# Performance work log

Measured on AMD Instinct MI355X. Metric: run time of the kernel, lower is better.

The kernel has to match this reference:

```python
import jax, jax.numpy as jnp
import numpy as np

N_NODES = 50000
N_EDGES = 1600000
IN_CH = 128
HID = 128
OUT_CH = 6
NUM_GRAPHS = 512


def _lin_params(key, fan_in, fan_out):
    k1, k2 = jax.random.split(key)
    bound = 1.0 / np.sqrt(fan_in)
    W = jax.random.uniform(k1, (fan_in, fan_out), minval=-bound, maxval=bound, dtype=jnp.float32)
    b = jax.random.uniform(k2, (fan_out,), minval=-bound, maxval=bound, dtype=jnp.float32)
    return W, b


def setup_inputs() -> dict:
    key = jax.random.key(0)
    ks = jax.random.split(key, 10)
    x = jax.random.normal(ks[0], (N_NODES, IN_CH), dtype=jnp.float32)
    edge_index = jax.random.randint(ks[1], (2, N_EDGES), 0, N_NODES, dtype=jnp.int64)
    batch = jnp.sort(jax.random.randint(ks[2], (N_NODES,), 0, NUM_GRAPHS, dtype=jnp.int64))
    W1a, b1a = _lin_params(ks[3], IN_CH, HID)
    W1b, b1b = _lin_params(ks[4], HID, HID)
    W2a, b2a = _lin_params(ks[5], HID, HID)
    W2b, b2b = _lin_params(ks[6], HID, HID)
    Wf1, bf1 = _lin_params(ks[7], HID, HID)
    Wf2, bf2 = _lin_params(ks[8], HID, OUT_CH)
    return {"x": x, "edge_index": edge_index, "batch": batch,
            "W1a": W1a, "b1a": b1a, "W1b": W1b, "b1b": b1b,
            "W2a": W2a, "b2a": b2a, "W2b": W2b, "b2b": b2b,
            "Wf1": Wf1, "bf1": bf1, "Wf2": Wf2, "bf2": bf2}


def _gin_conv(x, src, dst, Wa, ba, Wb, bb):
    # aggregate: sum of source-node features into target nodes (eps = 0)
    agg = jax.ops.segment_sum(x[src], dst, num_segments=N_NODES)
    h = x + agg  # (1 + eps) * x + sum_neighbors
    h = jax.nn.relu(h @ Wa + ba) @ Wb + bb  # 2-layer MLP (nn1/nn2)
    return h


def reference(x, edge_index, batch, W1a, b1a, W1b, b1b, W2a, b2a, W2b, b2b, Wf1, bf1, Wf2, bf2):
    src, dst = edge_index[0], edge_index[1]
    h = jax.nn.relu(_gin_conv(x, src, dst, W1a, b1a, W1b, b1b))
    h = jax.nn.relu(_gin_conv(h, src, dst, W2a, b2a, W2b, b2b))
    # global mean pool over graph ids
    sums = jax.ops.segment_sum(h, batch, num_segments=NUM_GRAPHS)  # [G, HID]
    counts = jax.ops.segment_sum(jnp.ones((h.shape[0],), h.dtype), batch, num_segments=NUM_GRAPHS)
    pooled = sums / jnp.maximum(counts, 1.0)[:, None]
    out = jax.nn.relu(pooled @ Wf1 + bf1) @ Wf2 + bf2  # [G, 6]
    return jax.nn.sigmoid(out)
```

## Files before the change

### kernel.cpp

```cpp
#include <hip/hip_runtime.h>

typedef unsigned short u16;
typedef unsigned int u32;

#define N_NODES 50000
#define N_EDGES 1600000
#define CH 128
#define CHW 64
#define NG 512
#define CAP 128
#define PAD 136
#define NBINS 196
#define BINCAP 12288
#define ECHUNK 1563

typedef __bf16 bf16x8 __attribute__((ext_vector_type(8)));
typedef float f32x4 __attribute__((ext_vector_type(4)));

#define OFF_DEG 0ull
#define OFF_BUCKET 200192ull
#define OFF_XB 13000192ull
#define OFF_HSUM 25800192ull
#define OFF_H1 38600192ull
#define OFF_GS 51400192ull
#define OFF_GE 51402240ull
#define OFF_BCUR 51404288ull
#define OFF_WT 51405312ull
#define OFF_BC 51536384ull
#define OFF_WF1 51538432ull
#define OFF_BF1 51603968ull
#define OFF_WF2 51604480ull
#define OFF_BF2 51607552ull

__device__ __forceinline__ float bflo(u32 v) { return __builtin_bit_cast(float, v << 16); }
__device__ __forceinline__ float bfhi(u32 v) { return __builtin_bit_cast(float, v & 0xffff0000u); }
__device__ __forceinline__ float bf2f(u16 v) { return __builtin_bit_cast(float, ((u32)v) << 16); }
__device__ __forceinline__ u16 f2bf(float f) {
    u32 x = __builtin_bit_cast(u32, f);
    x += 0x7fffu + ((x >> 16) & 1u);
    return (u16)(x >> 16);
}
__device__ __forceinline__ u32 pack2(float a, float b) {
    return (u32)f2bf(a) | ((u32)f2bf(b) << 16);
}
__device__ __forceinline__ bool probe_bf16(u32 w0) {
    u32 ex = (w0 >> 7) & 0xFFu;
    bool ok = ((w0 & 0x7FFFu) == 0u) || (ex >= 0x70u && ex <= 0x8Fu);
    return __popcll(__ballot(ok)) >= 48;
}
__device__ __forceinline__ float loadf(const void* p, int i, bool isbf) {
    return isbf ? bf2f(((const u16*)p)[i]) : ((const float*)p)[i];
}

__global__ __launch_bounds__(256) void fused_pre(char* ws, const u32* __restrict__ x,
                                                 u32* __restrict__ xb,
                                                 const int* __restrict__ ei,
                                                 const int* __restrict__ batch,
                                                 int* __restrict__ gstart, int* __restrict__ gend,
                                                 int* __restrict__ binCursor, u32* __restrict__ binned,
                                                 const void* W0, const void* W1,
                                                 const void* W2, const void* W3,
                                                 const void* b0, const void* b1,
                                                 const void* b2, const void* b3,
                                                 const void* Wf1, const void* bf1,
                                                 const void* Wf2, const void* bf2) {
    __shared__ __align__(16) char smem[33024];
    int tid = threadIdx.x, lane = tid & 63;
    int b = blockIdx.x;
    if (b < 8) {
        bool isbf = probe_bf16(((const u32*)W0)[lane]);
        int j = b >> 1, hf = b & 1;
        const void* src = (j == 0) ? W0 : (j == 1) ? W1 : (j == 2) ? W2 : W3;
        float* tile = (float*)smem;
        for (int it = 0; it < 32; ++it) {
            int idx = it * 256 + tid;
            int k = idx >> 7, n = idx & 127;
            tile[k * 129 + n] = loadf(src, (hf * 64 + k) * 128 + n, isbf);
        }
        __syncthreads();
        u16* Wt = (u16*)(ws + OFF_WT) + j * 16384;
        for (int it = 0; it < 32; ++it) {
            int o = it * 256 + tid;
            int n = o >> 6, kk = o & 63;
            Wt[n * 128 + hf * 64 + kk] = f2bf(tile[kk * 129 + n]);
        }
        return;
    }
    if (b < 78) {
        bool isbf = probe_bf16(((const u32*)W0)[lane]);
        int idx = (b - 8) * 256 + tid;
        float* bc = (float*)(ws + OFF_BC);
        float* Wf1c = (float*)(ws + OFF_WF1);
        float* bf1c = (float*)(ws + OFF_BF1);
        float* Wf2c = (float*)(ws + OFF_WF2);
        float* bf2c = (float*)(ws + OFF_BF2);
        if (idx < 512) {
            int j = idx >> 7, c = idx & 127;
            const void* src = (j == 0) ? b0 : (j == 1) ? b1 : (j == 2) ? b2 : b3;
            bc[idx] = loadf(src, c, isbf);
        } else if (idx < 16896) {
            Wf1c[idx - 512] = loadf(Wf1, idx - 512, isbf);
        } else if (idx < 17024) {
            bf1c[idx - 16896] = loadf(bf1, idx - 16896, isbf);
        } else if (idx < 17792) {
            Wf2c[idx - 17024] = loadf(Wf2, idx - 17024, isbf);
        } else if (idx < 17798) {
            bf2c[idx - 17792] = loadf(bf2, idx - 17792, isbf);
        }
        return;
    }
    if (b < 12578) {
        bool isbf = probe_bf16(x[lane]);
        int bb = b - 78;
        int i = bb * 256 + tid;
        if (isbf) {
            xb[i] = x[i];
        } else {
            float2 v = ((const float2*)x)[i];
            xb[i] = pack2(v.x, v.y);
        }
        if (bb < 196) {
            u32 hiw = ((const u32*)batch)[2 * (12500 + lane) + 1];
            bool i64 = __popcll(__ballot(hiw == 0u)) >= 48;
            int n = bb * 256 + tid;
            if (n < N_NODES) {
                int g = i64 ? batch[2 * n] : batch[n];
                atomicMin(&gstart[g], n);
                atomicMax(&gend[g], n + 1);
            }
        }
        return;
    }
    {
        int wg = b - 12578;
        u32* lhist = (u32*)smem;
        u32* lbase = lhist + 256;
        u32* lcur = lbase + 256;
        u32* stash = lcur + 256;
        u32 hiw = ((const u32*)ei)[2 * lane + 1];
        bool i64 = __popcll(__ballot(hiw == 0u)) >= 48;
        int e0 = wg * ECHUNK;
        int cnt = N_EDGES - e0; if (cnt > ECHUNK) cnt = ECHUNK; if (cnt < 0) cnt = 0;
        lhist[tid] = 0; lcur[tid] = 0;
        __syncthreads();
        for (int li = tid; li < cnt; li += 256) {
            int e = e0 + li;
            int s, d;
            if (i64) { s = ei[2 * e]; d = ei[2 * N_EDGES + 2 * e]; }
            else     { s = ei[e];     d = ei[N_EDGES + e]; }
            stash[li] = ((u32)d << 16) | (u32)s;
            atomicAdd(&lhist[d >> 8], 1u);
        }
        __syncthreads();
        u32 c = lhist[tid];
        if (c) lbase[tid] = (u32)atomicAdd(&binCursor[tid], (int)c);
        __syncthreads();
        for (int li = tid; li < cnt; li += 256) {
            u32 wv = stash[li];
            int bin = (int)(wv >> 24);
            u32 p = atomicAdd(&lcur[bin], 1u);
            binned[(size_t)bin * BINCAP + lbase[bin] + p] = wv;
        }
    }
}

__global__ __launch_bounds__(256) void fill_from_binned(const int* __restrict__ binCursor,
                                                        const u32* __restrict__ binned,
                                                        int* __restrict__ deg,
                                                        u16* __restrict__ bucket) {
    __shared__ u32 ldeg[256];
    int tid = threadIdx.x, b = blockIdx.x;
    int cnt = binCursor[b];
    ldeg[tid] = 0;
    __syncthreads();
    const u32* bp = binned + (size_t)b * BINCAP;
    for (int i = tid; i < cnt; i += 256) {
        u32 w = bp[i];
        u32 dl = (w >> 16) & 255u;
        u32 pos = atomicAdd(&ldeg[dl], 1u);
        if (pos < CAP) bucket[(size_t)(w >> 16) * CAP + pos] = (u16)(w & 0xFFFFu);
    }
    __syncthreads();
    int node = b * 256 + tid;
    if (node < N_NODES) deg[node] = (int)ldeg[tid];
}

__global__ __launch_bounds__(256) void agg_kernel(const u32* __restrict__ h,
                                                  const int* __restrict__ deg,
                                                  const u16* __restrict__ bucket,
                                                  u32* __restrict__ out) {
    int w = threadIdx.x >> 6, lane = threadIdx.x & 63;
    int node = blockIdx.x * 4 + w;
    if (node >= N_NODES) return;
    int sub = lane >> 4, q = lane & 15;
    const uint4* h4 = (const uint4*)h;
    float acc[8];
    {
        uint4 sv = make_uint4(0u, 0u, 0u, 0u);
        if (sub == 0) sv = h4[(size_t)node * 16 + q];
        acc[0] = bflo(sv.x); acc[1] = bfhi(sv.x);
        acc[2] = bflo(sv.y); acc[3] = bfhi(sv.y);
        acc[4] = bflo(sv.z); acc[5] = bfhi(sv.z);
        acc[6] = bflo(sv.w); acc[7] = bfhi(sv.w);
    }
    int d = deg[node];
    d = d > CAP ? CAP : d;
    const u32* bkw = (const u32*)(bucket + (size_t)node * CAP);
    const u32 sh = (u32)(sub & 1) * 16u;
    const int widx = sub >> 1;
    int j = 0;
    for (; j + 16 <= d; j += 16) {
        int base = j >> 1;
        u32 wd0 = bkw[base + widx];
        u32 wd1 = bkw[base + 2 + widx];
        u32 wd2 = bkw[base + 4 + widx];
        u32 wd3 = bkw[base + 6 + widx];
        uint4 v0 = h4[(size_t)((wd0 >> sh) & 0xFFFFu) * 16 + q];
        uint4 v1 = h4[(size_t)((wd1 >> sh) & 0xFFFFu) * 16 + q];
        uint4 v2 = h4[(size_t)((wd2 >> sh) & 0xFFFFu) * 16 + q];
        uint4 v3 = h4[(size_t)((wd3 >> sh) & 0xFFFFu) * 16 + q];
        acc[0] += bflo(v0.x) + bflo(v1.x) + bflo(v2.x) + bflo(v3.x);
        acc[1] += bfhi(v0.x) + bfhi(v1.x) + bfhi(v2.x) + bfhi(v3.x);
        acc[2] += bflo(v0.y) + bflo(v1.y) + bflo(v2.y) + bflo(v3.y);
        acc[3] += bfhi(v0.y) + bfhi(v1.y) + bfhi(v2.y) + bfhi(v3.y);
        acc[4] += bflo(v0.z) + bflo(v1.z) + bflo(v2.z) + bflo(v3.z);
        acc[5] += bfhi(v0.z) + bfhi(v1.z) + bfhi(v2.z) + bfhi(v3.z);
        acc[6] += bflo(v0.w) + bflo(v1.w) + bflo(v2.w) + bflo(v3.w);
        acc[7] += bfhi(v0.w) + bfhi(v1.w) + bfhi(v2.w) + bfhi(v3.w);
    }
    for (; j + 4 <= d; j += 4) {
        u32 wd = bkw[(j >> 1) + widx];
        uint4 v = h4[(size_t)((wd >> sh) & 0xFFFFu) * 16 + q];
        acc[0] += bflo(v.x); acc[1] += bfhi(v.x);
        acc[2] += bflo(v.y); acc[3] += bfhi(v.y);
        acc[4] += bflo(v.z); acc[5] += bfhi(v.z);
        acc[6] += bflo(v.w); acc[7] += bfhi(v.w);
    }
    if (j + sub < d) {
        int e = j + sub;
        u32 wd = bkw[e >> 1];
        u32 id = (wd >> ((u32)(e & 1) * 16u)) & 0xFFFFu;
        uint4 v = h4[(size_t)id * 16 + q];
        acc[0] += bflo(v.x); acc[1] += bfhi(v.x);
        acc[2] += bflo(v.y); acc[3] += bfhi(v.y);
        acc[4] += bflo(v.z); acc[5] += bfhi(v.z);
        acc[6] += bflo(v.w); acc[7] += bfhi(v.w);
    }
#pragma unroll
    for (int c = 0; c < 8; ++c) {
        acc[c] += __shfl_xor(acc[c], 16, 64);
        acc[c] += __shfl_xor(acc[c], 32, 64);
    }
    if (sub == 0) {
        uint4 o;
        o.x = pack2(acc[0], acc[1]);
        o.y = pack2(acc[2], acc[3]);
        o.z = pack2(acc[4], acc[5]);
        o.w = pack2(acc[6], acc[7]);
        ((uint4*)out)[(size_t)node * 16 + q] = o;
    }
}

__global__ __launch_bounds__(256) void mlp_kernel(const u16* __restrict__ in,
                                                  const u16* __restrict__ Wta,
                                                  const float* __restrict__ ba,
                                                  const u16* __restrict__ Wtb,
                                                  const float* __restrict__ bb,
                                                  u16* __restrict__ out,
                                                  int nrows) {
    __shared__ __align__(16) u16 Wlds[128 * PAD];
    __shared__ __align__(16) u16 tlds[64 * PAD];
    const int tid = threadIdx.x;
    const int w = tid >> 6;
    const int lane = tid & 63;
    const int n16 = lane & 15;
    const int quad = lane >> 4;
    const int row0 = blockIdx.x * 64 + w * 16;
    const bool active = row0 < nrows;

    {
        const uint4* wsrc = (const uint4*)Wta;
#pragma unroll
        for (int it = 0; it < 8; ++it) {
            int idx = tid + it * 256;
            int n = idx >> 4, c = idx & 15;
            *(uint4*)&Wlds[n * PAD + c * 8] = wsrc[idx];
        }
    }
    __syncthreads();

    f32x4 acc[8];
    bf16x8 afrag[4];
    if (active) {
        const u16* rowp = in + (size_t)(row0 + n16) * CH + quad * 8;
#pragma unroll
        for (int ks = 0; ks < 4; ++ks)
            afrag[ks] = *(const bf16x8*)(rowp + ks * 32);
#pragma unroll
        for (int ct = 0; ct < 8; ++ct) {
            f32x4 a = {0.f, 0.f, 0.f, 0.f};
#pragma unroll
            for (int ks = 0; ks < 4; ++ks) {
                bf16x8 b = *(const bf16x8*)&Wlds[(u32)(ct * 16 + n16) * PAD + ks * 32 + quad * 8];
                a = __builtin_amdgcn_mfma_f32_16x16x32_bf16(afrag[ks], b, a, 0, 0, 0);
            }
            acc[ct] = a;
        }
#pragma unroll
        for (int ct = 0; ct < 8; ++ct) {
            float bv = ba[ct * 16 + n16];
#pragma unroll
            for (int r = 0; r < 4; ++r) {
                float v = fmaxf(acc[ct][r] + bv, 0.f);
                tlds[(w * 16 + quad * 4 + r) * PAD + ct * 16 + n16] = f2bf(v);
            }
        }
    }
    __syncthreads();
    {
        const uint4* wsrc = (const uint4*)Wtb;
#pragma unroll
        for (int it = 0; it < 8; ++it) {
            int idx = tid + it * 256;
            int n = idx >> 4, c = idx & 15;
            *(uint4*)&Wlds[n * PAD + c * 8] = wsrc[idx];
        }
    }
    __syncthreads();

    if (active) {
#pragma unroll
        for (int ks = 0; ks < 4; ++ks)
            afrag[ks] = *(const bf16x8*)&tlds[(u32)(w * 16 + n16) * PAD + ks * 32 + quad * 8];
#pragma unroll
        for (int ct = 0; ct < 8; ++ct) {
            f32x4 a = {0.f, 0.f, 0.f, 0.f};
#pragma unroll
            for (int ks = 0; ks < 4; ++ks) {
                bf16x8 b = *(const bf16x8*)&Wlds[(u32)(ct * 16 + n16) * PAD + ks * 32 + quad * 8];
                a = __builtin_amdgcn_mfma_f32_16x16x32_bf16(afrag[ks], b, a, 0, 0, 0);
            }
            acc[ct] = a;
        }
#pragma unroll
        for (int ct = 0; ct < 8; ++ct) {
            float bv = bb[ct * 16 + n16];
#pragma unroll
            for (int r = 0; r < 4; ++r) {
                float v = fmaxf(acc[ct][r] + bv, 0.f);
                tlds[(w * 16 + quad * 4 + r) * PAD + ct * 16 + n16] = f2bf(v);
            }
        }
        u32* outw = (u32*)out;
        for (int r = 0; r < 16; ++r) {
            u32 v = *(const u32*)&tlds[(w * 16 + r) * PAD + lane * 2];
            outw[(size_t)(row0 + r) * CHW + lane] = v;
        }
    }
}

__global__ __launch_bounds__(256) void pool_final(const u32* __restrict__ h,
                                                  const int* __restrict__ gstart,
                                                  const int* __restrict__ gend,
                                                  const float* __restrict__ Wf1,
                                                  const float* __restrict__ bf1,
                                                  const float* __restrict__ Wf2,
                                                  const float* __restrict__ bf2v,
                                                  float* __restrict__ out) {
    __shared__ float rowb[4][128];
    __shared__ float tb[4][128];
    int w = threadIdx.x >> 6, lane = threadIdx.x & 63;
    int g = blockIdx.x * 4 + w;
    int sub = lane >> 4, q = lane & 15;
    int s = gstart[g], e = gend[g];
    const uint4* h4 = (const uint4*)h;
    float acc[8] = {0.f, 0.f, 0.f, 0.f, 0.f, 0.f, 0.f, 0.f};
    int i = s + sub;
    for (; i + 4 < e; i += 8) {
        uint4 v0 = h4[(size_t)i * 16 + q];
        uint4 v1 = h4[(size_t)(i + 4) * 16 + q];
        acc[0] += bflo(v0.x) + bflo(v1.x); acc[1] += bfhi(v0.x) + bfhi(v1.x);
        acc[2] += bflo(v0.y) + bflo(v1.y); acc[3] += bfhi(v0.y) + bfhi(v1.y);
        acc[4] += bflo(v0.z) + bflo(v1.z); acc[5] += bfhi(v0.z) + bfhi(v1.z);
        acc[6] += bflo(v0.w) + bflo(v1.w); acc[7] += bfhi(v0.w) + bfhi(v1.w);
    }
    for (; i < e; i += 4) {
        uint4 v = h4[(size_t)i * 16 + q];
        acc[0] += bflo(v.x); acc[1] += bfhi(v.x);
        acc[2] += bflo(v.y); acc[3] += bfhi(v.y);
        acc[4] += bflo(v.z); acc[5] += bfhi(v.z);
        acc[6] += bflo(v.w); acc[7] += bfhi(v.w);
    }
#pragma unroll
    for (int c = 0; c < 8; ++c) {
        acc[c] += __shfl_xor(acc[c], 16, 64);
        acc[c] += __shfl_xor(acc[c], 32, 64);
    }
    if (sub == 0) {
        float inv = 1.f / (float)((e - s) > 0 ? (e - s) : 1);
#pragma unroll
        for (int k = 0; k < 4; ++k) {
            rowb[w][(q * 4 + k) * 2] = acc[2 * k] * inv;
            rowb[w][(q * 4 + k) * 2 + 1] = acc[2 * k + 1] * inv;
        }
    }
    __syncthreads();
#pragma unroll
    for (int jj = 0; jj < 2; ++jj) {
        int jn = lane + jj * 64;
        float a = bf1[jn];
        for (int k = 0; k < 128; ++k) a += rowb[w][k] * Wf1[k * 128 + jn];
        tb[w][jn] = fmaxf(a, 0.f);
    }
    __syncthreads();
    if (lane < 6) {
        float a = bf2v[lane];
        for (int k = 0; k < 128; ++k) a += tb[w][k] * Wf2[k * 6 + lane];
        out[g * 6 + lane] = 1.f / (1.f + __expf(-a));
    }
}

extern "C" void kernel_launch(void* const* d_in, const int* in_sizes, int n_in,
                              void* d_out, int out_size, void* d_ws, size_t ws_size,
                              hipStream_t stream) {
    const u32* x = (const u32*)d_in[0];
    const int* ei = (const int*)d_in[1];
    const int* batch = (const int*)d_in[2];
    float* out = (float*)d_out;

    char* ws = (char*)d_ws;
    int* deg = (int*)(ws + OFF_DEG);
    u16* bucket = (u16*)(ws + OFF_BUCKET);
    u32* XB = (u32*)(ws + OFF_XB);
    u32* HSUM = (u32*)(ws + OFF_HSUM);
    u32* H1 = (u32*)(ws + OFF_H1);
    int* gstart = (int*)(ws + OFF_GS);
    int* gend = (int*)(ws + OFF_GE);
    int* binCursor = (int*)(ws + OFF_BCUR);
    u16* Wt = (u16*)(ws + OFF_WT);
    float* bc = (float*)(ws + OFF_BC);
    float* Wf1c = (float*)(ws + OFF_WF1);
    float* bf1c = (float*)(ws + OFF_BF1);
    float* Wf2c = (float*)(ws + OFF_WF2);
    float* bf2c = (float*)(ws + OFF_BF2);
    u32* binned = HSUM;

    hipMemsetAsync(gend, 0, 3072, stream);
    hipMemsetAsync(gstart, 0x7F, 2048, stream);

    fused_pre<<<13602, 256, 0, stream>>>(ws, x, XB, ei, batch, gstart, gend, binCursor, binned,
        d_in[3], d_in[5], d_in[7], d_in[9],
        d_in[4], d_in[6], d_in[8], d_in[10],
        d_in[11], d_in[12], d_in[13], d_in[14]);
    fill_from_binned<<<NBINS, 256, 0, stream>>>(binCursor, binned, deg, bucket);

    agg_kernel<<<(N_NODES + 3) / 4, 256, 0, stream>>>(XB, deg, bucket, HSUM);
    mlp_kernel<<<(N_NODES + 63) / 64, 256, 0, stream>>>((const u16*)HSUM, Wt, bc,
                                                        Wt + 16384, bc + 128, (u16*)H1, N_NODES);
    agg_kernel<<<(N_NODES + 3) / 4, 256, 0, stream>>>(H1, deg, bucket, HSUM);
    mlp_kernel<<<(N_NODES + 63) / 64, 256, 0, stream>>>((const u16*)HSUM, Wt + 32768, bc + 256,
                                                        Wt + 49152, bc + 384, (u16*)XB, N_NODES);
    pool_final<<<NG / 4, 256, 0, stream>>>(XB, gstart, gend, Wf1c, bf1c, Wf2c, bf2c, out);
}
```

Before: 309.6 us.

## Split fused preprocessing into separate kernels and pad bin cursors

Breaks the monolithic preprocessing kernel into three launches: small weight/bias conversion plus in-kernel init of cursors and graph bounds, x conversion with batch bounds (8 elements per thread), and edge binning. The two hipMemsetAsync calls are replaced by the init in the first kernel. Edge binning now uses 256 workgroups of 6250 edges with a larger LDS stash, and the global bin cursors are spaced 16 ints apart to reduce atomic contention and false sharing. This adds extra launches and gives up the concurrency of running all stages in one grid, in exchange for fewer memset calls, fewer global atomics per bin, and less per-block setup.

```diff
diff --git a/kernel.cpp b/kernel.cpp
--- a/kernel.cpp
+++ b/kernel.cpp
@@ -12,7 +12,9 @@
 #define PAD 136
 #define NBINS 196
 #define BINCAP 12288
-#define ECHUNK 1563
+#define NSCAT 256
+#define ECHUNK 6250
+#define CURS 16
 
 typedef __bf16 bf16x8 __attribute__((ext_vector_type(8)));
 typedef float f32x4 __attribute__((ext_vector_type(4)));
@@ -24,13 +26,13 @@
 #define OFF_H1 38600192ull
 #define OFF_GS 51400192ull
 #define OFF_GE 51402240ull
-#define OFF_BCUR 51404288ull
-#define OFF_WT 51405312ull
-#define OFF_BC 51536384ull
-#define OFF_WF1 51538432ull
-#define OFF_BF1 51603968ull
-#define OFF_WF2 51604480ull
-#define OFF_BF2 51607552ull
+#define OFF_WT 51404288ull
+#define OFF_BC 51535360ull
+#define OFF_WF1 51537408ull
+#define OFF_BF1 51602944ull
+#define OFF_WF2 51603456ull
+#define OFF_BF2 51606528ull
+#define OFF_BCUR 51606592ull
 
 __device__ __forceinline__ float bflo(u32 v) { return __builtin_bit_cast(float, v << 16); }
 __device__ __forceinline__ float bfhi(u32 v) { return __builtin_bit_cast(float, v & 0xffff0000u); }
@@ -52,26 +54,20 @@
     return isbf ? bf2f(((const u16*)p)[i]) : ((const float*)p)[i];
 }
 
-__global__ __launch_bounds__(256) void fused_pre(char* ws, const u32* __restrict__ x,
-                                                 u32* __restrict__ xb,
-                                                 const int* __restrict__ ei,
-                                                 const int* __restrict__ batch,
-                                                 int* __restrict__ gstart, int* __restrict__ gend,
-                                                 int* __restrict__ binCursor, u32* __restrict__ binned,
-                                                 const void* W0, const void* W1,
-                                                 const void* W2, const void* W3,
-                                                 const void* b0, const void* b1,
-                                                 const void* b2, const void* b3,
-                                                 const void* Wf1, const void* bf1,
-                                                 const void* Wf2, const void* bf2) {
-    __shared__ __align__(16) char smem[33024];
+__global__ __launch_bounds__(256) void prep_small(char* ws,
+                                                  const void* W0, const void* W1,
+                                                  const void* W2, const void* W3,
+                                                  const void* b0, const void* b1,
+                                                  const void* b2, const void* b3,
+                                                  const void* Wf1, const void* bf1,
+                                                  const void* Wf2, const void* bf2) {
+    __shared__ float tile[64 * 129];
     int tid = threadIdx.x, lane = tid & 63;
     int b = blockIdx.x;
     if (b < 8) {
         bool isbf = probe_bf16(((const u32*)W0)[lane]);
         int j = b >> 1, hf = b & 1;
         const void* src = (j == 0) ? W0 : (j == 1) ? W1 : (j == 2) ? W2 : W3;
-        float* tile = (float*)smem;
         for (int it = 0; it < 32; ++it) {
             int idx = it * 256 + tid;
             int k = idx >> 7, n = idx & 127;
@@ -109,58 +105,83 @@
         }
         return;
     }
-    if (b < 12578) {
-        bool isbf = probe_bf16(x[lane]);
-        int bb = b - 78;
-        int i = bb * 256 + tid;
-        if (isbf) {
-            xb[i] = x[i];
-        } else {
-            float2 v = ((const float2*)x)[i];
-            xb[i] = pack2(v.x, v.y);
-        }
-        if (bb < 196) {
-            u32 hiw = ((const u32*)batch)[2 * (12500 + lane) + 1];
-            bool i64 = __popcll(__ballot(hiw == 0u)) >= 48;
-            int n = bb * 256 + tid;
-            if (n < N_NODES) {
-                int g = i64 ? batch[2 * n] : batch[n];
-                atomicMin(&gstart[g], n);
-                atomicMax(&gend[g], n + 1);
+    {
+        int idx = (b - 78) * 256 + tid;
+        int* binCursor = (int*)(ws + OFF_BCUR);
+        int* gstart = (int*)(ws + OFF_GS);
+        int* gend = (int*)(ws + OFF_GE);
+        if (idx < NBINS * CURS) {
+            binCursor[idx] = 0;
+        } else if (idx < NBINS * CURS + 512) {
+            gstart[idx - NBINS * CURS] = 0x7FFFFFFF;
+        } else if (idx < NBINS * CURS + 1024) {
+            gend[idx - NBINS * CURS - 512] = 0;
+        }
+    }
+}
+
+__global__ __launch_bounds__(256) void cvt_gb(const u32* __restrict__ x, u32* __restrict__ xb,
+                                              const int* __restrict__ batch,
+                                              int* __restrict__ gstart,
+                                              int* __restrict__ gend) {
+    int tid = threadIdx.x, lane = tid & 63;
+    bool isbf = probe_bf16(x[lane]);
+    int base = blockIdx.x * 2048;
+#pragma unroll
+    for (int it = 0; it < 8; ++it) {
+        int i = base + it * 256 + tid;
+        if (i < N_NODES * CHW) {
+            if (isbf) {
+                xb[i] = x[i];
+            } else {
+                float2 v = ((const float2*)x)[i];
+                xb[i] = pack2(v.x, v.y);
             }
         }
-        return;
-    }
-    {
-        int wg = b - 12578;
-        u32* lhist = (u32*)smem;
-        u32* lbase = lhist + 256;
-        u32* lcur = lbase + 256;
-        u32* stash = lcur + 256;
-        u32 hiw = ((const u32*)ei)[2 * lane + 1];
+    }
+    if (blockIdx.x < 196) {
+        u32 hiw = ((const u32*)batch)[2 * (12500 + lane) + 1];
         bool i64 = __popcll(__ballot(hiw == 0u)) >= 48;
-        int e0 = wg * ECHUNK;
-        int cnt = N_EDGES - e0; if (cnt > ECHUNK) cnt = ECHUNK; if (cnt < 0) cnt = 0;
-        lhist[tid] = 0; lcur[tid] = 0;
-        __syncthreads();
-        for (int li = tid; li < cnt; li += 256) {
-            int e = e0 + li;
-            int s, d;
-            if (i64) { s = ei[2 * e]; d = ei[2 * N_EDGES + 2 * e]; }
-            else     { s = ei[e];     d = ei[N_EDGES + e]; }
-            stash[li] = ((u32)d << 16) | (u32)s;
-            atomicAdd(&lhist[d >> 8], 1u);
-        }
-        __syncthreads();
-        u32 c = lhist[tid];
-        if (c) lbase[tid] = (u32)atomicAdd(&binCursor[tid], (int)c);
-        __syncthreads();
-        for (int li = tid; li < cnt; li += 256) {
-            u32 wv = stash[li];
-            int bin = (int)(wv >> 24);
-            u32 p = atomicAdd(&lcur[bin], 1u);
-            binned[(size_t)bin * BINCAP + lbase[bin] + p] = wv;
-        }
+        int n = blockIdx.x * 256 + tid;
+        if (n < N_NODES) {
+            int g = i64 ? batch[2 * n] : batch[n];
+            atomicMin(&gstart[g], n);
+            atomicMax(&gend[g], n + 1);
+        }
+    }
+}
+
+__global__ __launch_bounds__(256) void edge_scatter(const int* __restrict__ ei,
+                                                    int* __restrict__ binCursor,
+                                                    u32* __restrict__ binned) {
+    __shared__ u32 lhist[256];
+    __shared__ u32 lbase[256];
+    __shared__ u32 lcur[256];
+    __shared__ u32 stash[ECHUNK];
+    int tid = threadIdx.x, wg = blockIdx.x;
+    int lane = tid & 63;
+    u32 hiw = ((const u32*)ei)[2 * lane + 1];
+    bool i64 = __popcll(__ballot(hiw == 0u)) >= 48;
+    int e0 = wg * ECHUNK;
+    lhist[tid] = 0; lcur[tid] = 0;
+    __syncthreads();
+    for (int li = tid; li < ECHUNK; li += 256) {
+        int e = e0 + li;
+        int s, d;
+        if (i64) { s = ei[2 * e]; d = ei[2 * N_EDGES + 2 * e]; }
+        else     { s = ei[e];     d = ei[N_EDGES + e]; }
+        stash[li] = ((u32)d << 16) | (u32)s;
+        atomicAdd(&lhist[d >> 8], 1u);
+    }
+    __syncthreads();
+    u32 c = lhist[tid];
+    if (c) lbase[tid] = (u32)atomicAdd(&binCursor[tid * CURS], (int)c);
+    __syncthreads();
+    for (int li = tid; li < ECHUNK; li += 256) {
+        u32 wv = stash[li];
+        int bin = (int)(wv >> 24);
+        u32 p = atomicAdd(&lcur[bin], 1u);
+        binned[(size_t)bin * BINCAP + lbase[bin] + p] = wv;
     }
 }
 
@@ -170,7 +191,7 @@
                                                         u16* __restrict__ bucket) {
     __shared__ u32 ldeg[256];
     int tid = threadIdx.x, b = blockIdx.x;
-    int cnt = binCursor[b];
+    int cnt = binCursor[b * CURS];
     ldeg[tid] = 0;
     __syncthreads();
     const u32* bp = binned + (size_t)b * BINCAP;
@@ -445,13 +466,12 @@
     float* bf2c = (float*)(ws + OFF_BF2);
     u32* binned = HSUM;
 
-    hipMemsetAsync(gend, 0, 3072, stream);
-    hipMemsetAsync(gstart, 0x7F, 2048, stream);
-
-    fused_pre<<<13602, 256, 0, stream>>>(ws, x, XB, ei, batch, gstart, gend, binCursor, binned,
+    prep_small<<<95, 256, 0, stream>>>(ws,
         d_in[3], d_in[5], d_in[7], d_in[9],
         d_in[4], d_in[6], d_in[8], d_in[10],
         d_in[11], d_in[12], d_in[13], d_in[14]);
+    cvt_gb<<<1563, 256, 0, stream>>>(x, XB, batch, gstart, gend);
+    edge_scatter<<<NSCAT, 256, 0, stream>>>(ei, binCursor, binned);
     fill_from_binned<<<NBINS, 256, 0, stream>>>(binCursor, binned, deg, bucket);
 
     agg_kernel<<<(N_NODES + 3) / 4, 256, 0, stream>>>(XB, deg, bucket, HSUM);
```

Result: slower. 318.6 us (+2.9%).
